# Kernel optimization log

Measured on AMD Instinct MI355X. Metric: run time of the kernel, lower is better.

The kernel has to match this reference:

```python
import jax, jax.numpy as jnp
import numpy as np


def _rbf_forward(batches, centers, beta, W, b):
    # Pairwise Euclidean distances via GEMM expansion instead of materializing
    # the O(n*K*dim) difference tensor the torch code builds.
    x2 = jnp.sum(batches * batches, axis=1, keepdims=True)          # [n, 1]
    c2 = jnp.sum(centers * centers, axis=1)                          # [K]
    xc = jnp.einsum('nd,kd->nk', batches, centers)                   # [n, K]
    d2 = jnp.maximum(x2 + c2[None, :] - 2.0 * xc, 0.0)               # [n, K]
    dist = jnp.sqrt(d2)
    radial = jnp.exp(-beta * dist)                                   # beta: [1, K]
    return radial @ W.T + b                                          # [n, num_class]


def setup_inputs() -> dict:
    key = jax.random.key(0)
    k1, k2, k3, k4, k5 = jax.random.split(key, 5)
    n, K, dim, num_class = 16384, 2048, 512, 10
    batches = jax.random.normal(k1, (n, dim), dtype=jnp.float32)
    centers = jax.random.normal(k2, (K, dim), dtype=jnp.float32)
    beta = jnp.full((1, K), 0.1, dtype=jnp.float32)  # torch init: ones/10
    W = jax.random.normal(k4, (num_class, K), dtype=jnp.float32) / np.sqrt(K)
    b = jax.random.normal(k5, (num_class,), dtype=jnp.float32) * 0.01
    return {"batches": batches, "centers": centers, "beta": beta, "W": W, "b": b}


def reference(batches, centers, beta, W, b):
    return _rbf_forward(batches, centers, beta, W, b)
```

## Files before the change

### kernel.cpp

```cpp
#include <hip/hip_runtime.h>
#include <hip/hip_bf16.h>
#include <stdint.h>

#define M_N  16384
#define K_C  2048
#define DIM  512
#define NCLS 10
#define NBN  16
#define NBM  (M_N / 128)
#define BK   32

typedef unsigned short u16;
typedef float  f32x4  __attribute__((ext_vector_type(4)));
typedef __bf16 bf16x8 __attribute__((ext_vector_type(8)));


__device__ __forceinline__ void async_ld16(const void* g, void* l) {
  __builtin_amdgcn_global_load_lds(
      (const __attribute__((address_space(1))) void*)g,
      (__attribute__((address_space(3))) void*)l,
      16, 0, 0);
}

__device__ __forceinline__ u16 f2bf_rne(float f) {
  uint32_t u = __float_as_uint(f);
  u += 0x7FFFu + ((u >> 16) & 1u);
  return (u16)(u >> 16);
}


#define NPREP ((M_N + K_C) / 4)

__global__ __launch_bounds__(256) void prep(
    const float4* __restrict__ batches, const float4* __restrict__ centers,
    const float* __restrict__ W,
    ushort4* __restrict__ Abf, ushort4* __restrict__ Bbf,
    float* __restrict__ x2, float* __restrict__ c2, u16* __restrict__ Wperm) {
  int b = blockIdx.x, t = threadIdx.x;
  if (b < NPREP) {
    int lane = t & 63;
    int rp = b * 4 + (t >> 6);
    const float4* src; ushort4* dst; float* sq; int row;
    if (rp < M_N) { src = batches; dst = Abf; sq = x2; row = rp; }
    else          { src = centers; dst = Bbf; sq = c2; row = rp - M_N; }
    float ss = 0.f;
#pragma unroll
    for (int i = 0; i < 2; ++i) {
      float4 v = src[(size_t)row * 128 + i * 64 + lane];
      ss += v.x * v.x + v.y * v.y + v.z * v.z + v.w * v.w;
      ushort4 o;
      o.x = f2bf_rne(v.x); o.y = f2bf_rne(v.y);
      o.z = f2bf_rne(v.z); o.w = f2bf_rne(v.w);
      dst[(size_t)row * 128 + i * 64 + lane] = o;
    }
    ss += __shfl_down(ss, 32);
    ss += __shfl_down(ss, 16);
    ss += __shfl_down(ss, 8);
    ss += __shfl_down(ss, 4);
    ss += __shfl_down(ss, 2);
    ss += __shfl_down(ss, 1);
    if (lane == 0) sq[row] = ss;
  } else {
    int wb = b - NPREP;
#pragma unroll
    for (int i = 0; i < 4; ++i) {
      int p = wb * 1024 + i * 256 + t;
      int cls = p >> 11, k = p & 2047;
      int bn = k >> 7, rem = k & 127;
      int h = (rem >> 6) & 1, rem2 = rem & 63;
      int tt = rem2 >> 5, qq = (rem2 >> 3) & 3, jj = rem2 & 7;
      int c = bn * 128 + h * 64 + (2 * tt + (jj >> 2)) * 16 + qq * 4 + (jj & 3);
      Wperm[p] = (cls < NCLS) ? f2bf_rne(W[cls * K_C + c]) : (u16)0;
    }
  }
}


__global__ __launch_bounds__(256, 4) void rbf_main(
    const u16* __restrict__ A,
    const u16* __restrict__ B,
    const float* __restrict__ x2,
    const float* __restrict__ c2,
    const float* __restrict__ beta,
    const u16* __restrict__ Wperm,
    float* __restrict__ partial) {
  __shared__ alignas(16) u16 As[2][128 * BK];
  __shared__ alignas(16) u16 Bs[2][128 * BK];

  const int tid  = threadIdx.x;
  const int lane = tid & 63;
  const int wid  = tid >> 6;
  const int bid = blockIdx.x;
  const int g = bid >> 3, r8 = bid & 7;
  const int bm = r8 * 16 + (g & 15);
  const int bn = g >> 4;
  const int row0 = bm * 128, col0 = bn * 128;
  const int wrC = (wid >> 1) * 64;
  const int wcB = (wid & 1) * 64;
  const int cls = lane & 15, q = lane >> 4;

  f32x4 acc[4][4] = {};

  const int srow = tid >> 2;
  const int schunk = (tid & 3) ^ ((tid >> 3) & 3);
  const u16* aG = A + (size_t)(row0 + srow) * DIM + schunk * 8;
  const u16* bG = B + (size_t)(col0 + srow) * DIM + schunk * 8;

#define FILL(buf, k0)                                          \
  {                                                            \
    async_ld16(aG + (k0),            &As[buf][0]    + tid * 8);\
    async_ld16(aG + (k0) + 64 * DIM, &As[buf][2048] + tid * 8);\
    async_ld16(bG + (k0),            &Bs[buf][0]    + tid * 8);\
    async_ld16(bG + (k0) + 64 * DIM, &Bs[buf][2048] + tid * 8);\
  }

  int offC[4], offB[4];
#pragma unroll
  for (int i = 0; i < 4; ++i) {
    int rrC = wrC + i * 16 + cls;
    offC[i] = rrC * BK + (q ^ ((rrC >> 1) & 3)) * 8;
    int rrB = wcB + i * 16 + cls;
    offB[i] = rrB * BK + (q ^ ((rrB >> 1) & 3)) * 8;
  }

  FILL(0, 0)
  for (int it = 0; it < 16; ++it) {
    __syncthreads();
    if (it < 15) FILL((it + 1) & 1, (it + 1) * BK)
    const u16* as_ = As[it & 1];
    const u16* bs_ = Bs[it & 1];
    bf16x8 cf[4], bfr[4];
#pragma unroll
    for (int mi = 0; mi < 4; ++mi)
      cf[mi] = *(const bf16x8*)(bs_ + offC[mi]);
#pragma unroll
    for (int ni = 0; ni < 4; ++ni)
      bfr[ni] = *(const bf16x8*)(as_ + offB[ni]);
#pragma unroll
    for (int mi = 0; mi < 4; ++mi)
#pragma unroll
      for (int ni = 0; ni < 4; ++ni)
        acc[mi][ni] = __builtin_amdgcn_mfma_f32_16x16x32_bf16(
            cf[mi], bfr[ni], acc[mi][ni], 0, 0, 0);
  }

  float x2v[4];
#pragma unroll
  for (int ni = 0; ni < 4; ++ni)
    x2v[ni] = x2[row0 + wcB + ni * 16 + cls];
#pragma unroll
  for (int mi = 0; mi < 4; ++mi) {
    int base = col0 + wrC + mi * 16 + q * 4;
    float4 cq = *(const float4*)(c2 + base);
    float4 bq = *(const float4*)(beta + base);
#pragma unroll
    for (int ni = 0; ni < 4; ++ni)
#pragma unroll
      for (int r = 0; r < 4; ++r) {
        float xc = acc[mi][ni][r];
        float d2 = fmaxf(x2v[ni] + cq[r] - 2.0f * xc, 0.0f);
        acc[mi][ni][r] = __expf(-bq[r] * sqrtf(d2));
      }
  }

  const int h = wid >> 1;
  f32x4 acc2[4] = {};
#pragma unroll
  for (int t = 0; t < 2; ++t) {
    bf16x8 wfr = *(const bf16x8*)(Wperm + (size_t)cls * K_C + col0 +
                                  h * 64 + t * 32 + q * 8);
#pragma unroll
    for (int ni = 0; ni < 4; ++ni) {
      bf16x8 pk;
#pragma unroll
      for (int r = 0; r < 4; ++r) {
        pk[r]     = (__bf16)acc[2 * t][ni][r];
        pk[4 + r] = (__bf16)acc[2 * t + 1][ni][r];
      }
      acc2[ni] = __builtin_amdgcn_mfma_f32_16x16x32_bf16(
          pk, wfr, acc2[ni], 0, 0, 0);
    }
  }

  f32x4* sumbuf = (f32x4*)As;
  __syncthreads();
  if (wid >= 2) {
#pragma unroll
    for (int ni = 0; ni < 4; ++ni)
      sumbuf[((wid - 2) * 4 + ni) * 64 + lane] = acc2[ni];
  }
  __syncthreads();
  if (wid < 2) {
#pragma unroll
    for (int ni = 0; ni < 4; ++ni) {
      acc2[ni] += sumbuf[(wid * 4 + ni) * 64 + lane];
#pragma unroll
      for (int r = 0; r < 4; ++r) {
        int gr = row0 + wid * 64 + ni * 16 + q * 4 + r;
        partial[((size_t)bn * M_N + gr) * 16 + cls] = acc2[ni][r];
      }
    }
  }
}


__global__ __launch_bounds__(256) void reduce_out(
    const float* __restrict__ partial, const float* __restrict__ b,
    float* __restrict__ out) {
  int t = threadIdx.x;
  int row = blockIdx.x * 64 + (t >> 2);
  int quad = t & 3;
  f32x4 v = {0.f, 0.f, 0.f, 0.f};
#pragma unroll
  for (int s = 0; s < NBN; ++s) {
    f32x4 p = __builtin_nontemporal_load(
        (const f32x4*)(partial + ((size_t)s * M_N + row) * 16 + quad * 4));
    v += p;
  }
  if (quad == 0) {
    float4 bq = *(const float4*)b;
    float* o = out + (size_t)row * NCLS;
    *(float2*)o       = {v.x + bq.x, v.y + bq.y};
    *(float2*)(o + 2) = {v.z + bq.z, v.w + bq.w};
  } else if (quad == 1) {
    float4 bq = *(const float4*)(b + 4);
    float* o = out + (size_t)row * NCLS + 4;
    *(float2*)o       = {v.x + bq.x, v.y + bq.y};
    *(float2*)(o + 2) = {v.z + bq.z, v.w + bq.w};
  } else if (quad == 2) {
    *(float2*)(out + (size_t)row * NCLS + 8) = {v.x + b[8], v.y + b[9]};
  }
}


extern "C" void kernel_launch(void* const* d_in, const int* in_sizes, int n_in,
                              void* d_out, int out_size, void* d_ws, size_t ws_size,
                              hipStream_t stream) {
  const float* batches = (const float*)d_in[0];
  const float* centers = (const float*)d_in[1];
  const float* beta    = (const float*)d_in[2];
  const float* W       = (const float*)d_in[3];
  const float* bias    = (const float*)d_in[4];
  float* out = (float*)d_out;

  char* ws = (char*)d_ws;
  u16*  Abf = (u16*)ws;
  u16*  Bbf = (u16*)(ws + (size_t)M_N * DIM * 2);
  float* x2 = (float*)(ws + (size_t)(M_N + K_C) * DIM * 2);
  float* c2 = x2 + M_N;
  u16*  Wpm = (u16*)(c2 + K_C);
  float* partial = (float*)((char*)Wpm + 16 * K_C * 2);

  prep<<<dim3(NPREP + 32), dim3(256), 0, stream>>>(
      (const float4*)batches, (const float4*)centers, W,
      (ushort4*)Abf, (ushort4*)Bbf, x2, c2, Wpm);
  rbf_main<<<dim3(NBN * NBM), dim3(256), 0, stream>>>(
      Abf, Bbf, x2, c2, beta, Wpm, partial);
  reduce_out<<<dim3(M_N / 64), dim3(256), 0, stream>>>(partial, bias, out);
}
```

Measured before the change: 137.3 us.

## Widen center tile to 256 per block, halving partial slices

Each block now covers 256 centers instead of 128. Each wave computes an 8x4 MFMA tile covering 128 centers by 64 rows, and the W permutation and reduction are adapted to match. This halves the number of blocks, the partial-sum slices written and read by the reduce kernel, and the redundant A-tile loads. The cost is higher register pressure (launch bounds lowered to 2 blocks per CU), larger LDS use and fewer blocks to fill the GPU.

```diff
diff --git a/kernel.cpp b/kernel.cpp
--- a/kernel.cpp
+++ b/kernel.cpp
@@ -6,8 +6,7 @@
 #define K_C  2048
 #define DIM  512
 #define NCLS 10
-#define NBN  16
-#define NBM  (M_N / 128)
+#define NSL  8
 #define BK   32
 
 typedef unsigned short u16;
@@ -66,17 +65,17 @@
     for (int i = 0; i < 4; ++i) {
       int p = wb * 1024 + i * 256 + t;
       int cls = p >> 11, k = p & 2047;
-      int bn = k >> 7, rem = k & 127;
-      int h = (rem >> 6) & 1, rem2 = rem & 63;
+      int bn = k >> 8, rem = k & 255;
+      int h = rem >> 7, rem2 = rem & 127;
       int tt = rem2 >> 5, qq = (rem2 >> 3) & 3, jj = rem2 & 7;
-      int c = bn * 128 + h * 64 + (2 * tt + (jj >> 2)) * 16 + qq * 4 + (jj & 3);
+      int c = bn * 256 + h * 128 + (2 * tt + (jj >> 2)) * 16 + qq * 4 + (jj & 3);
       Wperm[p] = (cls < NCLS) ? f2bf_rne(W[cls * K_C + c]) : (u16)0;
     }
   }
 }
 
 
-__global__ __launch_bounds__(256, 4) void rbf_main(
+__global__ __launch_bounds__(256, 2) void rbf_main(
     const u16* __restrict__ A,
     const u16* __restrict__ B,
     const float* __restrict__ x2,
@@ -85,7 +84,7 @@
     const u16* __restrict__ Wperm,
     float* __restrict__ partial) {
   __shared__ alignas(16) u16 As[2][128 * BK];
-  __shared__ alignas(16) u16 Bs[2][128 * BK];
+  __shared__ alignas(16) u16 Bs[2][256 * BK];
 
   const int tid  = threadIdx.x;
   const int lane = tid & 63;
@@ -94,33 +93,38 @@
   const int g = bid >> 3, r8 = bid & 7;
   const int bm = r8 * 16 + (g & 15);
   const int bn = g >> 4;
-  const int row0 = bm * 128, col0 = bn * 128;
-  const int wrC = (wid >> 1) * 64;
-  const int wcB = (wid & 1) * 64;
+  const int row0 = bm * 128, col0 = bn * 256;
+  const int wc = (wid & 1) * 128;
+  const int wb = (wid >> 1) * 64;
   const int cls = lane & 15, q = lane >> 4;
 
-  f32x4 acc[4][4] = {};
+  f32x4 acc[8][4] = {};
 
   const int srow = tid >> 2;
   const int schunk = (tid & 3) ^ ((tid >> 3) & 3);
   const u16* aG = A + (size_t)(row0 + srow) * DIM + schunk * 8;
   const u16* bG = B + (size_t)(col0 + srow) * DIM + schunk * 8;
 
-#define FILL(buf, k0)                                          \
-  {                                                            \
-    async_ld16(aG + (k0),            &As[buf][0]    + tid * 8);\
-    async_ld16(aG + (k0) + 64 * DIM, &As[buf][2048] + tid * 8);\
-    async_ld16(bG + (k0),            &Bs[buf][0]    + tid * 8);\
-    async_ld16(bG + (k0) + 64 * DIM, &Bs[buf][2048] + tid * 8);\
-  }
-
-  int offC[4], offB[4];
+#define FILL(buf, k0)                                            \
+  {                                                              \
+    async_ld16(aG + (k0),             &As[buf][0]    + tid * 8); \
+    async_ld16(aG + (k0) +  64 * DIM, &As[buf][2048] + tid * 8); \
+    async_ld16(bG + (k0),             &Bs[buf][0]    + tid * 8); \
+    async_ld16(bG + (k0) +  64 * DIM, &Bs[buf][2048] + tid * 8); \
+    async_ld16(bG + (k0) + 128 * DIM, &Bs[buf][4096] + tid * 8); \
+    async_ld16(bG + (k0) + 192 * DIM, &Bs[buf][6144] + tid * 8); \
+  }
+
+  int offC[8], offB[4];
+#pragma unroll
+  for (int i = 0; i < 8; ++i) {
+    int rr = wc + i * 16 + cls;
+    offC[i] = rr * BK + (q ^ ((rr >> 1) & 3)) * 8;
+  }
 #pragma unroll
   for (int i = 0; i < 4; ++i) {
-    int rrC = wrC + i * 16 + cls;
-    offC[i] = rrC * BK + (q ^ ((rrC >> 1) & 3)) * 8;
-    int rrB = wcB + i * 16 + cls;
-    offB[i] = rrB * BK + (q ^ ((rrB >> 1) & 3)) * 8;
+    int rr = wb + i * 16 + cls;
+    offB[i] = rr * BK + (q ^ ((rr >> 1) & 3)) * 8;
   }
 
   FILL(0, 0)
@@ -129,15 +133,15 @@
     if (it < 15) FILL((it + 1) & 1, (it + 1) * BK)
     const u16* as_ = As[it & 1];
     const u16* bs_ = Bs[it & 1];
-    bf16x8 cf[4], bfr[4];
-#pragma unroll
-    for (int mi = 0; mi < 4; ++mi)
+    bf16x8 cf[8], bfr[4];
+#pragma unroll
+    for (int mi = 0; mi < 8; ++mi)
       cf[mi] = *(const bf16x8*)(bs_ + offC[mi]);
 #pragma unroll
     for (int ni = 0; ni < 4; ++ni)
       bfr[ni] = *(const bf16x8*)(as_ + offB[ni]);
 #pragma unroll
-    for (int mi = 0; mi < 4; ++mi)
+    for (int mi = 0; mi < 8; ++mi)
 #pragma unroll
       for (int ni = 0; ni < 4; ++ni)
         acc[mi][ni] = __builtin_amdgcn_mfma_f32_16x16x32_bf16(
@@ -147,10 +151,10 @@
   float x2v[4];
 #pragma unroll
   for (int ni = 0; ni < 4; ++ni)
-    x2v[ni] = x2[row0 + wcB + ni * 16 + cls];
-#pragma unroll
-  for (int mi = 0; mi < 4; ++mi) {
-    int base = col0 + wrC + mi * 16 + q * 4;
+    x2v[ni] = x2[row0 + wb + ni * 16 + cls];
+#pragma unroll
+  for (int mi = 0; mi < 8; ++mi) {
+    int base = col0 + wc + mi * 16 + q * 4;
     float4 cq = *(const float4*)(c2 + base);
     float4 bq = *(const float4*)(beta + base);
 #pragma unroll
@@ -163,12 +167,12 @@
       }
   }
 
-  const int h = wid >> 1;
+  const int h = wid & 1;
   f32x4 acc2[4] = {};
 #pragma unroll
-  for (int t = 0; t < 2; ++t) {
+  for (int t = 0; t < 4; ++t) {
     bf16x8 wfr = *(const bf16x8*)(Wperm + (size_t)cls * K_C + col0 +
-                                  h * 64 + t * 32 + q * 8);
+                                  h * 128 + t * 32 + q * 8);
 #pragma unroll
     for (int ni = 0; ni < 4; ++ni) {
       bf16x8 pk;
@@ -184,19 +188,19 @@
 
   f32x4* sumbuf = (f32x4*)As;
   __syncthreads();
-  if (wid >= 2) {
+  if (h == 1) {
 #pragma unroll
     for (int ni = 0; ni < 4; ++ni)
-      sumbuf[((wid - 2) * 4 + ni) * 64 + lane] = acc2[ni];
+      sumbuf[((wid >> 1) * 4 + ni) * 64 + lane] = acc2[ni];
   }
   __syncthreads();
-  if (wid < 2) {
+  if (h == 0) {
 #pragma unroll
     for (int ni = 0; ni < 4; ++ni) {
-      acc2[ni] += sumbuf[(wid * 4 + ni) * 64 + lane];
+      acc2[ni] += sumbuf[((wid >> 1) * 4 + ni) * 64 + lane];
 #pragma unroll
       for (int r = 0; r < 4; ++r) {
-        int gr = row0 + wid * 64 + ni * 16 + q * 4 + r;
+        int gr = row0 + wb + ni * 16 + q * 4 + r;
         partial[((size_t)bn * M_N + gr) * 16 + cls] = acc2[ni][r];
       }
     }
@@ -212,7 +216,7 @@
   int quad = t & 3;
   f32x4 v = {0.f, 0.f, 0.f, 0.f};
 #pragma unroll
-  for (int s = 0; s < NBN; ++s) {
+  for (int s = 0; s < NSL; ++s) {
     f32x4 p = __builtin_nontemporal_load(
         (const f32x4*)(partial + ((size_t)s * M_N + row) * 16 + quad * 4));
     v += p;
@@ -254,7 +258,7 @@
   prep<<<dim3(NPREP + 32), dim3(256), 0, stream>>>(
       (const float4*)batches, (const float4*)centers, W,
       (ushort4*)Abf, (ushort4*)Bbf, x2, c2, Wpm);
-  rbf_main<<<dim3(NBN * NBM), dim3(256), 0, stream>>>(
+  rbf_main<<<dim3(8 * (M_N / 128)), dim3(256), 0, stream>>>(
       Abf, Bbf, x2, c2, beta, Wpm, partial);
   reduce_out<<<dim3(M_N / 64), dim3(256), 0, stream>>>(partial, bias, out);
 }
```

Measured after the change: 146.4 us. 6.6% more time.
